# Performance work log

Measured on AMD Instinct MI355X. Metric: run time of the kernel, lower is better.

The kernel has to match this reference:

```python
import jax, jax.numpy as jnp
import numpy as np

B, NBV, VD, A = 65536, 56, 7, 81
_BN_INV = np.float32(1.0 / np.sqrt(1.0 + 1e-5))  # eval-mode BN, running mean=0 var=1 (init state)


def _bn(x, g, b):
    # x: [B, C, F], per-channel affine over axis -2
    return x * (g * _BN_INV)[:, None] + b[:, None]


def _dpg(x, W, b, ng=8, ni=8):
    # DenseAndPartialGPool: first ng*ni feats -> grouped max+avg pool, rest -> relu(Linear)
    grp = x[..., : ng * ni].reshape(x.shape[:-1] + (ng, ni))
    dense = jax.nn.relu(x[..., ng * ni :] @ W + b)
    return jnp.concatenate([grp.max(-1), grp.mean(-1), dense], -1)


def setup_inputs() -> dict:
    key = jax.random.key(0)
    ks = iter(jax.random.split(key, 80))

    def W(si, so):
        return jax.random.normal(next(ks), (si, so), jnp.float32) * np.float32(1.0 / np.sqrt(si))

    def bias(n):
        return jnp.full((n,), 0.01, jnp.float32)

    inp = {}
    inp["input_data"] = jax.random.normal(next(ks), (B, NBV, VD), jnp.float32)
    inp["valid_actions"] = jax.random.randint(next(ks), (B, 1, A), 0, 2) > 0
    # dense2d_1
    inp["W1"], inp["b1"], inp["g1"], inp["be1"] = W(NBV, 128), bias(128), jnp.ones((7,), jnp.float32), jnp.zeros((7,), jnp.float32)
    inp["W2"], inp["b2"], inp["g2"], inp["be2"] = W(128, 128), bias(128), jnp.ones((7,), jnp.float32), jnp.zeros((7,), jnp.float32)
    inp["Wp1"], inp["bp1"] = W(64, 112), bias(112)
    inp["W3"], inp["b3"], inp["g3"], inp["be3"] = W(128, 128), bias(128), jnp.ones((7,), jnp.float32), jnp.zeros((7,), jnp.float32)
    inp["Wp2"], inp["bp2"] = W(64, 112), bias(112)
    inp["W4"], inp["b4"], inp["g4"], inp["be4"] = W(128, 128), bias(128), jnp.ones((7,), jnp.float32), jnp.zeros((7,), jnp.float32)
    inp["W5"], inp["b5"], inp["g5"], inp["be5"] = W(704, 512), bias(512), jnp.ones((1,), jnp.float32), jnp.zeros((1,), jnp.float32)
    inp["W6"], inp["b6"], inp["g6"], inp["be6"] = W(512, 256), bias(256), jnp.ones((1,), jnp.float32), jnp.zeros((1,), jnp.float32)
    inp["Wp4"], inp["bp4"] = W(192, 240), bias(240)
    inp["W7"], inp["b7"], inp["g7"], inp["be7"] = W(256, 256), bias(256), jnp.ones((1,), jnp.float32), jnp.zeros((1,), jnp.float32)
    inp["W8"], inp["b8"], inp["g8"], inp["be8"] = W(256, 256), bias(256), jnp.ones((1,), jnp.float32), jnp.zeros((1,), jnp.float32)
    inp["Wp5"], inp["bp5"] = W(192, 240), bias(240)
    inp["Wpi1"], inp["bpi1"] = W(256, 256), bias(256)
    inp["Wpi2"], inp["bpi2"] = W(256, A), bias(A)
    inp["Wv1"], inp["bv1"] = W(256, 256), bias(256)
    inp["Wv2"], inp["bv2"] = W(256, 1), bias(1)
    return inp


def reference(input_data, valid_actions, W1, b1, g1, be1, W2, b2, g2, be2, Wp1, bp1,
              W3, b3, g3, be3, Wp2, bp2, W4, b4, g4, be4,
              W5, b5, g5, be5, W6, b6, g6, be6, Wp4, bp4,
              W7, b7, g7, be7, W8, b8, g8, be8, Wp5, bp5,
              Wpi1, bpi1, Wpi2, bpi2, Wv1, bv1, Wv2, bv2):
    relu = jax.nn.relu
    x = jnp.transpose(input_data, (0, 2, 1))          # [B, 7, 56]
    x = relu(_bn(x @ W1 + b1, g1, be1))               # [B, 7, 128]
    x = relu(_bn(x @ W2 + b2, g2, be2))
    x = _dpg(x, Wp1, bp1)                             # [B, 7, 128]
    x = relu(_bn(x @ W3 + b3, g3, be3))
    x = _dpg(x, Wp2, bp2)
    x = relu(_bn(x @ W4 + b4, g4, be4))               # [B, 7, 128]
    # FlattenAndPartialGPool(64, 5)
    xb, xe = x[:, :, :64], x[:, :, 64:]
    first = xb[:, :5, :]                              # [B, 5, 64]
    n = x.shape[0]
    x = jnp.concatenate([first.max(1), first.mean(1),
                         xb[:, 5:, :].reshape(n, -1), xe.reshape(n, -1)], -1)[:, None, :]  # [B,1,704]
    x = relu(_bn(x @ W5 + b5, g5, be5))               # [B, 1, 512]
    x = relu(_bn(x @ W6 + b6, g6, be6))               # [B, 1, 256]
    x = _dpg(x, Wp4, bp4)
    x = relu(_bn(x @ W7 + b7, g7, be7))
    x = relu(_bn(x @ W8 + b8, g8, be8))
    x = _dpg(x, Wp5, bp5)                             # [B, 1, 256]
    v = jnp.tanh((x @ Wv1 + bv1) @ Wv2 + bv2)         # [B, 1, 1]
    pi = (x @ Wpi1 + bpi1) @ Wpi2 + bpi2              # [B, 1, A]
    pi = jnp.where(valid_actions, pi, jnp.float32(-1e8))
    return jax.nn.log_softmax(pi, axis=-1)[:, 0, :], v[:, 0, 0]
```

## Files before the change

kernel.cpp:

```cpp
#include <hip/hip_runtime.h>
#include <hip/hip_bf16.h>
#include <math.h>

#define BN_INV 0.99999500003749966f
#define NEG_BIG (-100000000.0f)

typedef __attribute__((ext_vector_type(8))) short s16x8;
typedef __attribute__((ext_vector_type(4))) float f32x4;

#define MFMA16(a,b,c) __builtin_amdgcn_mfma_f32_16x16x32_bf16(a,b,c,0,0,0)

__device__ __forceinline__ ushort f2b(float f){
  unsigned u = __builtin_bit_cast(unsigned, f);
  unsigned r = (u + 0x7FFFu + ((u>>16)&1u)) >> 16;
  return (ushort)r;
}
__device__ __forceinline__ float b2f(ushort h){
  unsigned u = ((unsigned)h)<<16; return __builtin_bit_cast(float, u);
}
__device__ __forceinline__ unsigned pk2(float a, float b){
  return (unsigned)f2b(a) | ((unsigned)f2b(b) << 16);
}

#define OFF_W1   0
#define OFF_W2   8192
#define OFF_W3   24576
#define OFF_W4   40960
#define OFF_WP1  57344
#define OFF_WP2  64512
#define OFF_W5   71680
#define OFF_W6   432128
#define OFF_WP4  563200
#define OFF_WP5  609280
#define OFF_W7   655360
#define OFF_W8   720896
#define OFF_WPI1 786432
#define OFF_WPI2 851968
#define OFF_WV1  876544
#define OFF_X    942080

struct PrepParams {
  const float* src[15];
  long long off[15];
  int K[15], N[15], Kp[15], Np[15];
  ushort* ws;
};

__global__ void prep_pack(PrepParams pp){
  const int wi = blockIdx.y;
  const int Kp = pp.Kp[wi], Np = pp.Np[wi], K = pp.K[wi], N = pp.N[wi];
  const int tot = Kp*Np;
  int idx = blockIdx.x*256 + threadIdx.x;
  if (idx >= tot) return;
  int n = idx / Kp, k = idx - n*Kp;
  const float* s = pp.src[wi];
  float v = (k < K && n < N) ? s[k*N + n] : 0.f;
  pp.ws[pp.off[wi] + idx] = f2b(v);
}

#define S1 136

struct P1 {
  const float* inp; const ushort* ws; ushort* xout;
  const float *b1,*g1,*be1,*b2,*g2,*be2,*bp1,*b3,*g3,*be3,*bp2,*b4,*g4,*be4;
};

template<int KT>
__device__ __forceinline__ void p1_mmS(const ushort* X, ushort* Y,
    const ushort* Wt, const int Kp, const float* bias,
    const float* g, const float* be, int t)
{
  const int l=t&63, w=t>>6, lo=l&15, hi=l>>4;
  const int n0 = w*16;
  s16x8 Aw[KT];
  const ushort* wr = Wt + (n0+lo)*Kp + hi*8;
  #pragma unroll
  for (int kt=0;kt<KT;kt++) Aw[kt] = *(const s16x8*)(wr + kt*32);
  const float4 bs = *(const float4*)(bias + n0 + hi*4);
  int j = lo % 7;
  #pragma unroll
  for (int mt=0; mt<7; mt++){
    const int row = mt*16 + lo;
    const ushort* xr = X + row*S1 + hi*8;
    f32x4 a = {0.f,0.f,0.f,0.f};
    #pragma unroll
    for (int kt=0;kt<KT;kt++){
      s16x8 bx = *(const s16x8*)(xr + kt*32);
      a = MFMA16(Aw[kt], bx, a);
    }
    const float scj = g[j]*BN_INV, bbj = be[j];
    float v0 = fmaxf((a[0]+bs.x)*scj + bbj, 0.f);
    float v1 = fmaxf((a[1]+bs.y)*scj + bbj, 0.f);
    float v2 = fmaxf((a[2]+bs.z)*scj + bbj, 0.f);
    float v3 = fmaxf((a[3]+bs.w)*scj + bbj, 0.f);
    uint2 pv; pv.x = pk2(v0,v1); pv.y = pk2(v2,v3);
    *(uint2*)(Y + row*S1 + n0 + hi*4) = pv;
    j += 2; if (j >= 7) j -= 7;
  }
}

__device__ __forceinline__ void p1_dpgS(const ushort* X, ushort* Y,
    const ushort* Wpt, const float* bp, int t)
{
  const int l=t&63, w=t>>6, lo=l&15, hi=l>>4;
  #pragma unroll
  for (int it=0; it<2; it++){
    int idx = t + it*512;
    if (idx < 896){
      int row = idx>>3, gg = idx&7;
      s16x8 v8 = *(const s16x8*)(X + row*S1 + gg*8);
      float mx = b2f((ushort)v8[0]), sm = mx;
      #pragma unroll
      for (int q=1;q<8;q++){ float vv=b2f((ushort)v8[q]); mx=fmaxf(mx,vv); sm+=vv; }
      Y[row*S1+gg]   = f2b(mx);
      Y[row*S1+8+gg] = f2b(sm*0.125f);
    }
  }
  if (w < 7){
    const int n0 = w*16;
    const ushort* wr = Wpt + (n0+lo)*64 + hi*8;
    s16x8 Aw0 = *(const s16x8*)(wr);
    s16x8 Aw1 = *(const s16x8*)(wr + 32);
    const float4 bs = *(const float4*)(bp + n0 + hi*4);
    #pragma unroll
    for (int mt=0; mt<7; mt++){
      const int row = mt*16 + lo;
      const ushort* xr = X + row*S1 + 64 + hi*8;
      f32x4 a = {0.f,0.f,0.f,0.f};
      a = MFMA16(Aw0, *(const s16x8*)(xr), a);
      a = MFMA16(Aw1, *(const s16x8*)(xr+32), a);
      float v0 = fmaxf(a[0]+bs.x, 0.f);
      float v1 = fmaxf(a[1]+bs.y, 0.f);
      float v2 = fmaxf(a[2]+bs.z, 0.f);
      float v3 = fmaxf(a[3]+bs.w, 0.f);
      uint2 pv; pv.x = pk2(v0,v1); pv.y = pk2(v2,v3);
      *(uint2*)(Y + row*S1 + 16 + n0 + hi*4) = pv;
    }
  }
}

__global__ __launch_bounds__(512,4) void p1_kernel(P1 P){
  __shared__ ushort sA[112*S1];
  __shared__ ushort sB[112*S1];
  const int t = threadIdx.x;
  const size_t b0 = (size_t)blockIdx.x*16;
  {
    const int e = t>>5, la = t&31;
    const float* ep = P.inp + (b0+e)*392;
    ushort* dst = sA + e*7*S1;
    for (int i=la; i<56; i+=32){
      const float* q = ep + i*7;
      #pragma unroll
      for (int j=0;j<7;j++) dst[j*S1 + i] = f2b(q[j]);
    }
  }
  for (int idx=t; idx<896; idx+=512)
    sA[(idx>>3)*S1 + 56 + (idx&7)] = 0;
  __syncthreads();
  p1_mmS<2>(sA,sB, P.ws+OFF_W1, 64,  P.b1,P.g1,P.be1, t); __syncthreads();
  p1_mmS<4>(sB,sA, P.ws+OFF_W2, 128, P.b2,P.g2,P.be2, t); __syncthreads();
  p1_dpgS(sA,sB, P.ws+OFF_WP1, P.bp1, t);                 __syncthreads();
  p1_mmS<4>(sB,sA, P.ws+OFF_W3, 128, P.b3,P.g3,P.be3, t); __syncthreads();
  p1_dpgS(sA,sB, P.ws+OFF_WP2, P.bp2, t);                 __syncthreads();
  p1_mmS<4>(sB,sA, P.ws+OFF_W4, 128, P.b4,P.g4,P.be4, t); __syncthreads();
  ushort* xo = P.xout + b0*704;
  for (int idx=t; idx<896; idx+=512){
    int e = idx/56, ch = idx - e*56;
    int q = ch*8;
    const ushort* Xr = sA + e*7*S1;
    *(s16x8*)(xo + e*704 + 256 + q) = *(const s16x8*)(Xr + (q>>6)*S1 + 64 + (q&63));
  }
  for (int idx=t; idx<4096; idx+=512){
    int e = idx>>8, c = idx&255;
    const ushort* Xr = sA + e*7*S1;
    float v;
    if (c < 64){
      float mx = b2f(Xr[c]);
      #pragma unroll
      for (int j=1;j<5;j++) mx = fmaxf(mx, b2f(Xr[j*S1+c]));
      v = mx;
    } else if (c < 128){
      int cc = c-64; float sm = 0.f;
      #pragma unroll
      for (int j=0;j<5;j++) sm += b2f(Xr[j*S1+cc]);
      v = sm*0.2f;
    } else if (c < 192) v = b2f(Xr[5*S1 + c-128]);
    else                v = b2f(Xr[6*S1 + c-192]);
    xo[e*704 + c] = f2b(v);
  }
}

#define SY 520
#define SZ 264

struct P2 {
  const ushort* x; const ushort* ws; const void* valid;
  const float *b5,*g5,*be5,*b6,*g6,*be6,*bp4,*b7,*g7,*be7,*b8,*g8,*be8,*bp5;
  const float *bpi1,*bpi2,*bv1,*Wv2,*bv2;
  float* out; long long Btot;
};

template<int KT, int NTW, int MODE>
__device__ __forceinline__ void p2_mmS(const ushort* X, int sx, int xoff,
    ushort* Y, int sy, int yoff, const ushort* Wt, int Kp, int n0, int nact,
    const float* bias, int bmax, float sc, float bb, int lo, int hi)
{
  const ushort* xr0 = X + (0*16+lo)*sx + xoff + hi*8;
  const ushort* xr1 = X + (1*16+lo)*sx + xoff + hi*8;
  const ushort* wr[NTW];
  #pragma unroll
  for (int n=0;n<NTW;n++) wr[n] = Wt + (size_t)(n0+n*16+lo)*Kp + hi*8;
  f32x4 acc[2][NTW];
  #pragma unroll
  for (int m=0;m<2;m++)
    #pragma unroll
    for (int n=0;n<NTW;n++) acc[m][n] = (f32x4){0.f,0.f,0.f,0.f};
  #pragma unroll
  for (int kt=0; kt<KT; kt++){
    s16x8 bx0 = *(const s16x8*)(xr0 + kt*32);
    s16x8 bx1 = *(const s16x8*)(xr1 + kt*32);
    #pragma unroll
    for (int n=0;n<NTW;n++){
      if (n < nact){
        s16x8 aw = *(const s16x8*)(wr[n] + kt*32);
        acc[0][n] = MFMA16(aw, bx0, acc[0][n]);
        acc[1][n] = MFMA16(aw, bx1, acc[1][n]);
      }
    }
  }
  #pragma unroll
  for (int n=0;n<NTW;n++){
    if (n < nact){
      const int nc = n0 + n*16 + hi*4;
      float4 bs;
      if (nc+3 < bmax) bs = *(const float4*)(bias + nc);
      else {
        bs.x = (nc   < bmax)? bias[nc]  :0.f;
        bs.y = (nc+1 < bmax)? bias[nc+1]:0.f;
        bs.z = (nc+2 < bmax)? bias[nc+2]:0.f;
        bs.w = (nc+3 < bmax)? bias[nc+3]:0.f;
      }
      #pragma unroll
      for (int m=0;m<2;m++){
        const int row = m*16 + lo;
        float v0 = acc[m][n][0]+bs.x, v1 = acc[m][n][1]+bs.y;
        float v2 = acc[m][n][2]+bs.z, v3 = acc[m][n][3]+bs.w;
        if (MODE==0){
          v0 = fmaxf(v0*sc+bb,0.f); v1 = fmaxf(v1*sc+bb,0.f);
          v2 = fmaxf(v2*sc+bb,0.f); v3 = fmaxf(v3*sc+bb,0.f);
        } else if (MODE==1){
          v0 = fmaxf(v0,0.f); v1 = fmaxf(v1,0.f);
          v2 = fmaxf(v2,0.f); v3 = fmaxf(v3,0.f);
        }
        if (MODE==3){
          float4 fv = {v0,v1,v2,v3};
          *(float4*)((float*)Y + (size_t)row*sy + yoff + nc) = fv;
        } else {
          uint2 pv; pv.x = pk2(v0,v1); pv.y = pk2(v2,v3);
          *(uint2*)(Y + row*sy + yoff + nc) = pv;
        }
      }
    }
  }
}

__device__ __forceinline__ void p2_group(const ushort* X, ushort* Y, int t){
  int row = t>>3, gg = t&7;
  s16x8 v8 = *(const s16x8*)(X + row*SZ + gg*8);
  float mx = b2f((ushort)v8[0]), sm = mx;
  #pragma unroll
  for (int q=1;q<8;q++){ float vv = b2f((ushort)v8[q]); mx = fmaxf(mx,vv); sm += vv; }
  Y[row*SZ + gg]     = f2b(mx);
  Y[row*SZ + 8 + gg] = f2b(sm*0.125f);
}

__global__ __launch_bounds__(512,4) void p2_kernel(P2 P){
  __shared__ ushort sm[25344];
  __shared__ int sflags[2];
  ushort* A1 = sm;
  ushort* B1 = sm;
  ushort* C  = sm + 8448;
  ushort* B0 = sm + 16896;
  float*  Lf = (float*)(sm + 16896);
  const int t = threadIdx.x;
  const int l = t&63, w = t>>6, lo = l&15, hi = l>>4;
  const size_t b0 = (size_t)blockIdx.x * 32;

  if (t < 2) sflags[t] = 0;
  __syncthreads();
  if (t < 256){
    const unsigned* vw = (const unsigned*)P.valid;
    int f3=0, nz=0;
    #pragma unroll
    for (int i=0;i<4;i++){
      unsigned u = vw[t*4+i];
      if (u & 0xFFFFFF00u) nz=1;
      if (((u>>24)&0xFFu)==0x3Fu || ((u>>16)&0xFFu)==0x3Fu ||
          ((u>>8)&0xFFu)==0x3Fu  || (u&0xFFu)==0x3Fu) f3=1;
    }
    if (f3) atomicOr(&sflags[0],1);
    if (nz) atomicOr(&sflags[1],1);
  }
  p2_mmS<22,4,0>(P.x + b0*704, 704, 0, A1, SY, 0, P.ws+OFF_W5, 704,
                 w*64, 4, P.b5, 512, P.g5[0]*BN_INV, P.be5[0], lo,hi);
  __syncthreads();
  p2_mmS<16,2,0>(A1, SY, 0, B0, SZ, 0, P.ws+OFF_W6, 512,
                 w*32, 2, P.b6, 256, P.g6[0]*BN_INV, P.be6[0], lo,hi);
  __syncthreads();
  if (t < 256) p2_group(B0, B1, t);
  p2_mmS<6,2,1>(B0, SZ, 64, B1, SZ, 16, P.ws+OFF_WP4, 192,
                w*32, (w<7)?2:1, P.bp4, 240, 0.f,0.f, lo,hi);
  __syncthreads();
  p2_mmS<8,2,0>(B1, SZ, 0, B0, SZ, 0, P.ws+OFF_W7, 256,
                w*32, 2, P.b7, 256, P.g7[0]*BN_INV, P.be7[0], lo,hi);
  __syncthreads();
  p2_mmS<8,2,0>(B0, SZ, 0, B1, SZ, 0, P.ws+OFF_W8, 256,
                w*32, 2, P.b8, 256, P.g8[0]*BN_INV, P.be8[0], lo,hi);
  __syncthreads();
  if (t < 256) p2_group(B1, B0, t);
  p2_mmS<6,2,1>(B1, SZ, 64, B0, SZ, 16, P.ws+OFF_WP5, 192,
                w*32, (w<7)?2:1, P.bp5, 240, 0.f,0.f, lo,hi);
  __syncthreads();
  p2_mmS<8,2,2>(B0, SZ, 0, B1, SZ, 0, P.ws+OFF_WPI1, 256,
                w*32, 2, P.bpi1, 256, 0.f,0.f, lo,hi);
  p2_mmS<8,2,2>(B0, SZ, 0, C , SZ, 0, P.ws+OFF_WV1 , 256,
                w*32, 2, P.bv1 , 256, 0.f,0.f, lo,hi);
  __syncthreads();
  const int vmode = sflags[0] ? 2 : (sflags[1] ? 0 : 1);
  if (w < 6){
    p2_mmS<8,1,3>(B1, SZ, 0, (ushort*)Lf, 104, 0, P.ws+OFF_WPI2, 256,
                  w*16, 1, P.bpi2, 81, 0.f,0.f, lo,hi);
  } else if (w == 6){
    int row = l>>1, half = l&1;
    const ushort* hv = C + row*SZ + half*128;
    float s = 0.f;
    for (int k=0;k<128;k++) s += b2f(hv[k]) * P.Wv2[half*128+k];
    s += __shfl_xor(s, 1);
    if (!half) P.out[(size_t)P.Btot*81 + b0 + row] = tanhf(s + P.bv2[0]);
  }
  __syncthreads();
  if (t < 256){
    int row = t>>3, q = t&7;
    size_t b = b0 + row;
    const float* lr = Lf + row*104;
    float pm[11]; float mx = -INFINITY;
    #pragma unroll
    for (int i=0;i<11;i++){
      int c = q + 8*i;
      float v = NEG_BIG;
      if (c < 81){
        float sv = lr[c];
        bool valid;
        size_t vidx = b*81 + c;
        if (vmode==0)      valid = ((const unsigned char*)P.valid)[vidx] != 0;
        else if (vmode==1) valid = ((const int*)P.valid)[vidx] != 0;
        else               valid = ((const float*)P.valid)[vidx] != 0.f;
        v = valid ? sv : NEG_BIG;
      }
      pm[i] = v;
      mx = fmaxf(mx, v);
    }
    #pragma unroll
    for (int o=4;o;o>>=1) mx = fmaxf(mx, __shfl_xor(mx, o));
    float se = 0.f;
    #pragma unroll
    for (int i=0;i<11;i++){
      int c = q + 8*i;
      if (c < 81) se += expf(pm[i]-mx);
    }
    #pragma unroll
    for (int o=4;o;o>>=1) se += __shfl_xor(se, o);
    float lse = mx + logf(se);
    #pragma unroll
    for (int i=0;i<11;i++){
      int c = q + 8*i;
      if (c < 81) P.out[b*81 + c] = pm[i] - lse;
    }
  }
}

struct Params {
  const float* input;
  const void*  valid;
  const float *W1,*b1,*g1,*be1, *W2,*b2,*g2,*be2, *Wp1,*bp1;
  const float *W3,*b3,*g3,*be3, *Wp2,*bp2, *W4,*b4,*g4,*be4;
  const float *W5,*b5,*g5,*be5, *W6,*b6,*g6,*be6, *Wp4,*bp4;
  const float *W7,*b7,*g7,*be7, *W8,*b8,*g8,*be8, *Wp5,*bp5;
  const float *Wpi1,*bpi1,*Wpi2,*bpi2, *Wv1,*bv1,*Wv2,*bv2;
  float* out;
};

template<int K>
__device__ __forceinline__ void mm_p1(const float* __restrict__ X, float* __restrict__ Y,
    const float* __restrict__ W, const float* __restrict__ bias,
    const float* __restrict__ g, const float* __restrict__ be){
  const int t = threadIdx.x;
  const int m = t & 31, e = t >> 5;
  const int c0 = m * 4;
  const float* Xr = X + e*7*128;
  float acc[7][4];
  #pragma unroll
  for (int j=0;j<7;j++){acc[j][0]=0.f;acc[j][1]=0.f;acc[j][2]=0.f;acc[j][3]=0.f;}
  for (int k=0;k<K;k+=4){
    float4 wv[4];
    #pragma unroll
    for (int kk=0;kk<4;kk++) wv[kk] = *(const float4*)(W + (k+kk)*128 + c0);
    #pragma unroll
    for (int j=0;j<7;j++){
      float4 xv = *(const float4*)(Xr + j*128 + k);
      float xx[4] = {xv.x, xv.y, xv.z, xv.w};
      #pragma unroll
      for (int kk=0;kk<4;kk++){
        acc[j][0] += xx[kk]*wv[kk].x; acc[j][1] += xx[kk]*wv[kk].y;
        acc[j][2] += xx[kk]*wv[kk].z; acc[j][3] += xx[kk]*wv[kk].w;
      }
    }
  }
  float4 bs = *(const float4*)(bias + c0);
  #pragma unroll
  for (int j=0;j<7;j++){
    float sc = g[j]*BN_INV; float bb = be[j];
    float4 o;
    o.x = fmaxf((acc[j][0]+bs.x)*sc + bb, 0.f);
    o.y = fmaxf((acc[j][1]+bs.y)*sc + bb, 0.f);
    o.z = fmaxf((acc[j][2]+bs.z)*sc + bb, 0.f);
    o.w = fmaxf((acc[j][3]+bs.w)*sc + bb, 0.f);
    *(float4*)(Y + (e*7+j)*128 + c0) = o;
  }
}

__device__ __forceinline__ void dpg_p1f(const float* __restrict__ X, float* __restrict__ Y,
    const float* __restrict__ Wp, const float* __restrict__ bp){
  const int t = threadIdx.x;
  const int m = t & 31, e = t >> 5;
  const float* Xr = X + e*7*128;
  float* Yr = Y + e*7*128;
  if (m < 28) {
    const int c0 = m*4;
    float acc[7][4];
    #pragma unroll
    for (int j=0;j<7;j++){acc[j][0]=0.f;acc[j][1]=0.f;acc[j][2]=0.f;acc[j][3]=0.f;}
    for (int k=0;k<64;k+=4){
      float4 wv[4];
      #pragma unroll
      for (int kk=0;kk<4;kk++) wv[kk] = *(const float4*)(Wp + (k+kk)*112 + c0);
      #pragma unroll
      for (int j=0;j<7;j++){
        float4 xv = *(const float4*)(Xr + j*128 + 64 + k);
        float xx[4] = {xv.x, xv.y, xv.z, xv.w};
        #pragma unroll
        for (int kk=0;kk<4;kk++){
          acc[j][0] += xx[kk]*wv[kk].x; acc[j][1] += xx[kk]*wv[kk].y;
          acc[j][2] += xx[kk]*wv[kk].z; acc[j][3] += xx[kk]*wv[kk].w;
        }
      }
    }
    float4 bs = *(const float4*)(bp + c0);
    #pragma unroll
    for (int j=0;j<7;j++){
      float4 o;
      o.x = fmaxf(acc[j][0]+bs.x, 0.f); o.y = fmaxf(acc[j][1]+bs.y, 0.f);
      o.z = fmaxf(acc[j][2]+bs.z, 0.f); o.w = fmaxf(acc[j][3]+bs.w, 0.f);
      *(float4*)(Yr + j*128 + 16 + c0) = o;
    }
  } else if (m < 30) {
    #pragma unroll
    for (int j=0;j<7;j++){
      #pragma unroll
      for (int gi=0; gi<4; gi++){
        int gg = (m-28)*4 + gi;
        const float* p = Xr + j*128 + gg*8;
        float mx = p[0], smv = p[0];
        #pragma unroll
        for (int i=1;i<8;i++){ float v = p[i]; mx = fmaxf(mx, v); smv += v; }
        Yr[j*128 + gg] = mx;
        Yr[j*128 + 8 + gg] = smv*0.125f;
      }
    }
  }
}

__device__ __forceinline__ void flatten_st(const float* __restrict__ X, float* __restrict__ F){
  const int t = threadIdx.x, m = t & 31, e = t >> 5;
  const float* Xr = X + e*7*128;
  float* Fr = F + e*704;
  for (int col=m; col<704; col+=32){
    float v;
    if (col < 64){
      float mx = Xr[col];
      #pragma unroll
      for (int j=1;j<5;j++) mx = fmaxf(mx, Xr[j*128+col]);
      v = mx;
    } else if (col < 128){
      int c = col-64; float smv = 0.f;
      #pragma unroll
      for (int j=0;j<5;j++) smv += Xr[j*128+c];
      v = smv*0.2f;
    } else if (col < 192){ v = Xr[5*128 + (col-128)];
    } else if (col < 256){ v = Xr[6*128 + (col-192)];
    } else { int q = col-256; v = Xr[(q>>6)*128 + 64 + (q&63)]; }
    Fr[col] = v;
  }
}

template<int K, int N, int RPG, int MODE>
__device__ __forceinline__ void mm_p2(const float* __restrict__ X, int sx,
    float* __restrict__ Y, int sy, const float* __restrict__ W,
    const float* __restrict__ bias, float sc, float bb){
  constexpr int NC4 = N/4;
  constexpr int NG  = (8 + RPG - 1) / RPG;
  const int t = threadIdx.x;
  const int ci = t % NC4;
  const int grp = t / NC4;
  if (grp < NG) {
    const int c0 = ci*4;
    const int r0 = grp*RPG;
    float acc[RPG][4];
    #pragma unroll
    for (int r=0;r<RPG;r++){acc[r][0]=0.f;acc[r][1]=0.f;acc[r][2]=0.f;acc[r][3]=0.f;}
    for (int k=0;k<K;k+=4){
      float4 wv[4];
      #pragma unroll
      for (int kk=0;kk<4;kk++) wv[kk] = *(const float4*)(W + (k+kk)*N + c0);
      #pragma unroll
      for (int r=0;r<RPG;r++){
        float4 xv = *(const float4*)(X + (r0+r)*sx + k);
        float xx[4] = {xv.x, xv.y, xv.z, xv.w};
        #pragma unroll
        for (int kk=0;kk<4;kk++){
          acc[r][0] += xx[kk]*wv[kk].x; acc[r][1] += xx[kk]*wv[kk].y;
          acc[r][2] += xx[kk]*wv[kk].z; acc[r][3] += xx[kk]*wv[kk].w;
        }
      }
    }
    float4 bs = *(const float4*)(bias + c0);
    #pragma unroll
    for (int r=0;r<RPG;r++){
      float o[4] = {acc[r][0]+bs.x, acc[r][1]+bs.y, acc[r][2]+bs.z, acc[r][3]+bs.w};
      #pragma unroll
      for (int q=0;q<4;q++){
        if (MODE == 0) o[q] = o[q]*sc + bb;
        if (MODE <= 1) o[q] = fmaxf(o[q], 0.f);
      }
      float4 ov = {o[0],o[1],o[2],o[3]};
      *(float4*)(Y + (r0+r)*sy + c0) = ov;
    }
  }
}

__device__ __forceinline__ void dpg_p2_group(const float* __restrict__ X, float* __restrict__ Y){
  const int t = threadIdx.x;
  if (t < 128){
    int r = t >> 4, g0 = t & 15;
    const float* p = X + r*256 + (g0&7)*8;
    float mx = p[0], smv = p[0];
    #pragma unroll
    for (int i=1;i<8;i++){ float v = p[i]; mx = fmaxf(mx, v); smv += v; }
    Y[r*256 + g0] = (g0 < 8) ? mx : smv*0.125f;
  }
}

__global__ __launch_bounds__(256, 2)
void splendor_fwd(Params P, int Bt)
{
  __shared__ float bufA[7168];
  __shared__ float bufB[7168];
  __shared__ int sflags[2];
  const int t = threadIdx.x;
  const int b0 = blockIdx.x * 8;

  if (t < 2) sflags[t] = 0;
  __syncthreads();
  {
    const unsigned int* vw = (const unsigned int*)P.valid;
    int f3 = 0, nz = 0;
    #pragma unroll
    for (int i=0;i<4;i++){
      unsigned int u = vw[t*4 + i];
      if (u & 0xFFFFFF00u) nz = 1;
      if (((u>>24)&0xFFu)==0x3Fu || ((u>>16)&0xFFu)==0x3Fu ||
          ((u>>8)&0xFFu)==0x3Fu  || (u&0xFFu)==0x3Fu) f3 = 1;
    }
    if (f3) atomicOr(&sflags[0], 1);
    if (nz) atomicOr(&sflags[1], 1);
  }
  {
    const float* inp = P.input + (size_t)b0*392;
    for (int f=t; f<3136; f+=256){
      int e = f/392, rem = f - e*392;
      int i = rem/7, j = rem - i*7;
      bufA[(e*7+j)*128 + i] = inp[f];
    }
  }
  __syncthreads();
  const int vmode = sflags[0] ? 2 : (sflags[1] ? 0 : 1);

  mm_p1<56>(bufA, bufB, P.W1, P.b1, P.g1, P.be1);   __syncthreads();
  mm_p1<128>(bufB, bufA, P.W2, P.b2, P.g2, P.be2);  __syncthreads();
  dpg_p1f(bufA, bufB, P.Wp1, P.bp1);                __syncthreads();
  mm_p1<128>(bufB, bufA, P.W3, P.b3, P.g3, P.be3);  __syncthreads();
  dpg_p1f(bufA, bufB, P.Wp2, P.bp2);                __syncthreads();
  mm_p1<128>(bufB, bufA, P.W4, P.b4, P.g4, P.be4);  __syncthreads();
  flatten_st(bufA, bufB);                           __syncthreads();

  mm_p2<704,512,4,0>(bufB,704, bufA,512, P.W5, P.b5, P.g5[0]*BN_INV, P.be5[0]); __syncthreads();
  mm_p2<512,256,2,0>(bufA,512, bufB,256, P.W6, P.b6, P.g6[0]*BN_INV, P.be6[0]); __syncthreads();
  mm_p2<192,240,2,1>(bufB+64,256, bufA+16,256, P.Wp4, P.bp4, 0.f, 0.f);
  dpg_p2_group(bufB, bufA);                         __syncthreads();
  mm_p2<256,256,2,0>(bufA,256, bufB,256, P.W7, P.b7, P.g7[0]*BN_INV, P.be7[0]); __syncthreads();
  mm_p2<256,256,2,0>(bufB,256, bufA,256, P.W8, P.b8, P.g8[0]*BN_INV, P.be8[0]); __syncthreads();
  mm_p2<192,240,2,1>(bufA+64,256, bufB+16,256, P.Wp5, P.bp5, 0.f, 0.f);
  dpg_p2_group(bufA, bufB);                         __syncthreads();
  mm_p2<256,256,2,2>(bufB,256, bufA,256,      P.Wpi1, P.bpi1, 0.f, 0.f);
  mm_p2<256,256,2,2>(bufB,256, bufA+2048,256, P.Wv1,  P.bv1,  0.f, 0.f);
  __syncthreads();

  {
    const int r = t >> 5, lq = t & 31;
    const int b = b0 + r;
    const float* hp = bufA + r*256;
    float pm[3] = {NEG_BIG, NEG_BIG, NEG_BIG};
    float mx = -INFINITY;
    #pragma unroll
    for (int p=0;p<3;p++){
      int c = lq + 32*p;
      if (c < 81){
        float s = P.bpi2[c];
        for (int k=0;k<256;k++) s += hp[k]*P.Wpi2[k*81+c];
        bool valid;
        size_t idx = (size_t)b*81 + c;
        if (vmode == 0)      valid = ((const unsigned char*)P.valid)[idx] != 0;
        else if (vmode == 1) valid = ((const int*)P.valid)[idx] != 0;
        else                 valid = ((const float*)P.valid)[idx] != 0.f;
        pm[p] = valid ? s : NEG_BIG;
        mx = fmaxf(mx, pm[p]);
      }
    }
    #pragma unroll
    for (int off=16;off;off>>=1) mx = fmaxf(mx, __shfl_xor(mx, off, 32));
    float se = 0.f;
    #pragma unroll
    for (int p=0;p<3;p++){
      int c = lq + 32*p;
      if (c < 81) se += expf(pm[p]-mx);
    }
    #pragma unroll
    for (int off=16;off;off>>=1) se += __shfl_xor(se, off, 32);
    float lse = mx + logf(se);
    #pragma unroll
    for (int p=0;p<3;p++){
      int c = lq + 32*p;
      if (c < 81) P.out[(size_t)b*81 + c] = pm[p]-lse;
    }
  }
  if (t < 8){
    const float* hv = bufA + 2048 + t*256;
    float s = P.bv2[0];
    for (int k=0;k<256;k++) s += hv[k]*P.Wv2[k];
    P.out[(size_t)Bt*81 + b0 + t] = tanhf(s);
  }
}

extern "C" void kernel_launch(void* const* d_in, const int* in_sizes, int n_in,
                              void* d_out, int out_size, void* d_ws, size_t ws_size,
                              hipStream_t stream)
{
  const float* input = (const float*)d_in[0];
  const void*  valid = d_in[1];
  const float* W1  = (const float*)d_in[2];  const float* b1  = (const float*)d_in[3];
  const float* g1  = (const float*)d_in[4];  const float* be1 = (const float*)d_in[5];
  const float* W2  = (const float*)d_in[6];  const float* b2  = (const float*)d_in[7];
  const float* g2  = (const float*)d_in[8];  const float* be2 = (const float*)d_in[9];
  const float* Wp1 = (const float*)d_in[10]; const float* bp1 = (const float*)d_in[11];
  const float* W3  = (const float*)d_in[12]; const float* b3  = (const float*)d_in[13];
  const float* g3  = (const float*)d_in[14]; const float* be3 = (const float*)d_in[15];
  const float* Wp2 = (const float*)d_in[16]; const float* bp2 = (const float*)d_in[17];
  const float* W4  = (const float*)d_in[18]; const float* b4  = (const float*)d_in[19];
  const float* g4  = (const float*)d_in[20]; const float* be4 = (const float*)d_in[21];
  const float* W5  = (const float*)d_in[22]; const float* b5  = (const float*)d_in[23];
  const float* g5  = (const float*)d_in[24]; const float* be5 = (const float*)d_in[25];
  const float* W6  = (const float*)d_in[26]; const float* b6  = (const float*)d_in[27];
  const float* g6  = (const float*)d_in[28]; const float* be6 = (const float*)d_in[29];
  const float* Wp4 = (const float*)d_in[30]; const float* bp4 = (const float*)d_in[31];
  const float* W7  = (const float*)d_in[32]; const float* b7  = (const float*)d_in[33];
  const float* g7  = (const float*)d_in[34]; const float* be7 = (const float*)d_in[35];
  const float* W8  = (const float*)d_in[36]; const float* b8  = (const float*)d_in[37];
  const float* g8  = (const float*)d_in[38]; const float* be8 = (const float*)d_in[39];
  const float* Wp5 = (const float*)d_in[40]; const float* bp5 = (const float*)d_in[41];
  const float* Wpi1= (const float*)d_in[42]; const float* bpi1= (const float*)d_in[43];
  const float* Wpi2= (const float*)d_in[44]; const float* bpi2= (const float*)d_in[45];
  const float* Wv1 = (const float*)d_in[46]; const float* bv1 = (const float*)d_in[47];
  const float* Wv2 = (const float*)d_in[48]; const float* bv2 = (const float*)d_in[49];

  const long long Bt = in_sizes[0] / 392;
  const size_t need = ((size_t)OFF_X + (size_t)Bt*704) * 2;

  if (ws_size >= need && (Bt % 32) == 0) {
    ushort* wsu = (ushort*)d_ws;
    PrepParams pp;
    const float* srcs[15] = {W1,W2,W3,W4,Wp1,Wp2,W5,W6,Wp4,Wp5,W7,W8,Wpi1,Wpi2,Wv1};
    const long long offs[15] = {OFF_W1,OFF_W2,OFF_W3,OFF_W4,OFF_WP1,OFF_WP2,OFF_W5,OFF_W6,
                                OFF_WP4,OFF_WP5,OFF_W7,OFF_W8,OFF_WPI1,OFF_WPI2,OFF_WV1};
    const int Ks[15]  = {56,128,128,128, 64, 64,704,512,192,192,256,256,256,256,256};
    const int Ns[15]  = {128,128,128,128,112,112,512,256,240,240,256,256,256, 81,256};
    const int Kps[15] = {64,128,128,128, 64, 64,704,512,192,192,256,256,256,256,256};
    const int Nps[15] = {128,128,128,128,112,112,512,256,240,240,256,256,256, 96,256};
    for (int i=0;i<15;i++){
      pp.src[i]=srcs[i]; pp.off[i]=offs[i];
      pp.K[i]=Ks[i]; pp.N[i]=Ns[i]; pp.Kp[i]=Kps[i]; pp.Np[i]=Nps[i];
    }
    pp.ws = wsu;
    hipLaunchKernelGGL(prep_pack, dim3(1408,15), dim3(256), 0, stream, pp);

    P1 p1;
    p1.inp = input; p1.ws = wsu; p1.xout = wsu + OFF_X;
    p1.b1=b1; p1.g1=g1; p1.be1=be1; p1.b2=b2; p1.g2=g2; p1.be2=be2; p1.bp1=bp1;
    p1.b3=b3; p1.g3=g3; p1.be3=be3; p1.bp2=bp2; p1.b4=b4; p1.g4=g4; p1.be4=be4;
    hipLaunchKernelGGL(p1_kernel, dim3((unsigned)(Bt/16)), dim3(512), 0, stream, p1);

    P2 p2;
    p2.x = wsu + OFF_X; p2.ws = wsu; p2.valid = valid;
    p2.b5=b5; p2.g5=g5; p2.be5=be5; p2.b6=b6; p2.g6=g6; p2.be6=be6; p2.bp4=bp4;
    p2.b7=b7; p2.g7=g7; p2.be7=be7; p2.b8=b8; p2.g8=g8; p2.be8=be8; p2.bp5=bp5;
    p2.bpi1=bpi1; p2.bpi2=bpi2; p2.bv1=bv1; p2.Wv2=Wv2; p2.bv2=bv2;
    p2.out = (float*)d_out; p2.Btot = Bt;
    hipLaunchKernelGGL(p2_kernel, dim3((unsigned)(Bt/32)), dim3(512), 0, stream, p2);
  } else {
    Params P;
    P.input = input; P.valid = valid;
    P.W1=W1; P.b1=b1; P.g1=g1; P.be1=be1; P.W2=W2; P.b2=b2; P.g2=g2; P.be2=be2;
    P.Wp1=Wp1; P.bp1=bp1; P.W3=W3; P.b3=b3; P.g3=g3; P.be3=be3; P.Wp2=Wp2; P.bp2=bp2;
    P.W4=W4; P.b4=b4; P.g4=g4; P.be4=be4; P.W5=W5; P.b5=b5; P.g5=g5; P.be5=be5;
    P.W6=W6; P.b6=b6; P.g6=g6; P.be6=be6; P.Wp4=Wp4; P.bp4=bp4;
    P.W7=W7; P.b7=b7; P.g7=g7; P.be7=be7; P.W8=W8; P.b8=b8; P.g8=g8; P.be8=be8;
    P.Wp5=Wp5; P.bp5=bp5; P.Wpi1=Wpi1; P.bpi1=bpi1; P.Wpi2=Wpi2; P.bpi2=bpi2;
    P.Wv1=Wv1; P.bv1=bv1; P.Wv2=Wv2; P.bv2=bv2;
    P.out = (float*)d_out;
    hipLaunchKernelGGL(splendor_fwd, dim3((unsigned)(Bt/8)), dim3(256), 0, stream, P, (int)Bt);
  }
}
```

Baseline: 890.4 us.

## Halve p2 block to 4 waves with wider per-wave N tiles and staged X in LDS

Cuts the second-stage kernel from 512 to 256 threads per block, so each wave computes twice as many output columns (NTW doubled) and reuses each loaded activation fragment across more MFMAs. The W5 input tile is now copied from global into padded shared memory (stride 712) before the first GEMM, instead of being read directly from global per wave. LDS use grows to about 79 KB, which lowers occupancy (launch bounds 256,2), and each wave holds more accumulators, which raises register pressure. Weight pointer arithmetic is simplified to a single base pointer.

```diff
diff --git a/kernel.cpp b/kernel.cpp
--- a/kernel.cpp
+++ b/kernel.cpp
@@ -190,8 +190,10 @@
   }
 }
 
-#define SY 520
-#define SZ 264
+#define SXS 712
+#define SYS 520
+#define SZ  264
+#define SLF 104
 
 struct P2 {
   const ushort* x; const ushort* ws; const void* valid;
@@ -205,11 +207,9 @@
     ushort* Y, int sy, int yoff, const ushort* Wt, int Kp, int n0, int nact,
     const float* bias, int bmax, float sc, float bb, int lo, int hi)
 {
-  const ushort* xr0 = X + (0*16+lo)*sx + xoff + hi*8;
-  const ushort* xr1 = X + (1*16+lo)*sx + xoff + hi*8;
-  const ushort* wr[NTW];
-  #pragma unroll
-  for (int n=0;n<NTW;n++) wr[n] = Wt + (size_t)(n0+n*16+lo)*Kp + hi*8;
+  const ushort* xr0 = X + lo*sx + xoff + hi*8;
+  const ushort* xr1 = xr0 + 16*sx;
+  const ushort* wr  = Wt + (size_t)(n0+lo)*Kp + hi*8;
   f32x4 acc[2][NTW];
   #pragma unroll
   for (int m=0;m<2;m++)
@@ -222,7 +222,7 @@
     #pragma unroll
     for (int n=0;n<NTW;n++){
       if (n < nact){
-        s16x8 aw = *(const s16x8*)(wr[n] + kt*32);
+        s16x8 aw = *(const s16x8*)(wr + (size_t)n*16*Kp + kt*32);
         acc[0][n] = MFMA16(aw, bx0, acc[0][n]);
         acc[1][n] = MFMA16(aw, bx1, acc[1][n]);
       }
@@ -274,21 +274,22 @@
   Y[row*SZ + 8 + gg] = f2b(sm*0.125f);
 }
 
-__global__ __launch_bounds__(512,4) void p2_kernel(P2 P){
-  __shared__ ushort sm[25344];
+__global__ __launch_bounds__(256,2) void p2_kernel(P2 P){
+  __shared__ ushort sm2[39680];
   __shared__ int sflags[2];
-  ushort* A1 = sm;
-  ushort* B1 = sm;
-  ushort* C  = sm + 8448;
-  ushort* B0 = sm + 16896;
-  float*  Lf = (float*)(sm + 16896);
+  ushort* xs = sm2;
+  ushort* ys = sm2 + 22784;
+  ushort* B0 = sm2;
+  ushort* B1 = sm2 + 8448;
+  float*  Lf = (float*)(sm2 + 16896);
+  ushort* C  = sm2 + 31232;
   const int t = threadIdx.x;
   const int l = t&63, w = t>>6, lo = l&15, hi = l>>4;
   const size_t b0 = (size_t)blockIdx.x * 32;
 
   if (t < 2) sflags[t] = 0;
   __syncthreads();
-  if (t < 256){
+  {
     const unsigned* vw = (const unsigned*)P.valid;
     int f3=0, nz=0;
     #pragma unroll
@@ -301,36 +302,44 @@
     if (f3) atomicOr(&sflags[0],1);
     if (nz) atomicOr(&sflags[1],1);
   }
-  p2_mmS<22,4,0>(P.x + b0*704, 704, 0, A1, SY, 0, P.ws+OFF_W5, 704,
-                 w*64, 4, P.b5, 512, P.g5[0]*BN_INV, P.be5[0], lo,hi);
-  __syncthreads();
-  p2_mmS<16,2,0>(A1, SY, 0, B0, SZ, 0, P.ws+OFF_W6, 512,
-                 w*32, 2, P.b6, 256, P.g6[0]*BN_INV, P.be6[0], lo,hi);
-  __syncthreads();
-  if (t < 256) p2_group(B0, B1, t);
-  p2_mmS<6,2,1>(B0, SZ, 64, B1, SZ, 16, P.ws+OFF_WP4, 192,
-                w*32, (w<7)?2:1, P.bp4, 240, 0.f,0.f, lo,hi);
-  __syncthreads();
-  p2_mmS<8,2,0>(B1, SZ, 0, B0, SZ, 0, P.ws+OFF_W7, 256,
-                w*32, 2, P.b7, 256, P.g7[0]*BN_INV, P.be7[0], lo,hi);
-  __syncthreads();
-  p2_mmS<8,2,0>(B0, SZ, 0, B1, SZ, 0, P.ws+OFF_W8, 256,
-                w*32, 2, P.b8, 256, P.g8[0]*BN_INV, P.be8[0], lo,hi);
-  __syncthreads();
-  if (t < 256) p2_group(B1, B0, t);
-  p2_mmS<6,2,1>(B1, SZ, 64, B0, SZ, 16, P.ws+OFF_WP5, 192,
-                w*32, (w<7)?2:1, P.bp5, 240, 0.f,0.f, lo,hi);
-  __syncthreads();
-  p2_mmS<8,2,2>(B0, SZ, 0, B1, SZ, 0, P.ws+OFF_WPI1, 256,
-                w*32, 2, P.bpi1, 256, 0.f,0.f, lo,hi);
-  p2_mmS<8,2,2>(B0, SZ, 0, C , SZ, 0, P.ws+OFF_WV1 , 256,
-                w*32, 2, P.bv1 , 256, 0.f,0.f, lo,hi);
+  {
+    const ushort* xi = P.x + b0*704;
+    for (int ci = t; ci < 32*88; ci += 256){
+      int row = ci/88, c8 = ci - row*88;
+      *(s16x8*)(xs + row*SXS + c8*8) = *(const s16x8*)(xi + row*704 + c8*8);
+    }
+  }
+  __syncthreads();
+  p2_mmS<22,8,0>(xs, SXS, 0, ys, SYS, 0, P.ws+OFF_W5, 704,
+                 w*128, 8, P.b5, 512, P.g5[0]*BN_INV, P.be5[0], lo,hi);
+  __syncthreads();
+  p2_mmS<16,4,0>(ys, SYS, 0, B0, SZ, 0, P.ws+OFF_W6, 512,
+                 w*64, 4, P.b6, 256, P.g6[0]*BN_INV, P.be6[0], lo,hi);
+  __syncthreads();
+  p2_group(B0, B1, t);
+  p2_mmS<6,4,1>(B0, SZ, 64, B1, SZ, 16, P.ws+OFF_WP4, 192,
+                w*64, (w<3)?4:3, P.bp4, 240, 0.f,0.f, lo,hi);
+  __syncthreads();
+  p2_mmS<8,4,0>(B1, SZ, 0, B0, SZ, 0, P.ws+OFF_W7, 256,
+                w*64, 4, P.b7, 256, P.g7[0]*BN_INV, P.be7[0], lo,hi);
+  __syncthreads();
+  p2_mmS<8,4,0>(B0, SZ, 0, B1, SZ, 0, P.ws+OFF_W8, 256,
+                w*64, 4, P.b8, 256, P.g8[0]*BN_INV, P.be8[0], lo,hi);
+  __syncthreads();
+  p2_group(B1, B0, t);
+  p2_mmS<6,4,1>(B1, SZ, 64, B0, SZ, 16, P.ws+OFF_WP5, 192,
+                w*64, (w<3)?4:3, P.bp5, 240, 0.f,0.f, lo,hi);
+  __syncthreads();
+  p2_mmS<8,4,2>(B0, SZ, 0, B1, SZ, 0, P.ws+OFF_WPI1, 256,
+                w*64, 4, P.bpi1, 256, 0.f,0.f, lo,hi);
+  p2_mmS<8,4,2>(B0, SZ, 0, C , SZ, 0, P.ws+OFF_WV1 , 256,
+                w*64, 4, P.bv1 , 256, 0.f,0.f, lo,hi);
   __syncthreads();
   const int vmode = sflags[0] ? 2 : (sflags[1] ? 0 : 1);
-  if (w < 6){
-    p2_mmS<8,1,3>(B1, SZ, 0, (ushort*)Lf, 104, 0, P.ws+OFF_WPI2, 256,
-                  w*16, 1, P.bpi2, 81, 0.f,0.f, lo,hi);
-  } else if (w == 6){
+  if (w < 3){
+    p2_mmS<8,2,3>(B1, SZ, 0, (ushort*)Lf, SLF, 0, P.ws+OFF_WPI2, 256,
+                  w*32, 2, P.bpi2, 81, 0.f,0.f, lo,hi);
+  } else {
     int row = l>>1, half = l&1;
     const ushort* hv = C + row*SZ + half*128;
     float s = 0.f;
@@ -339,10 +348,10 @@
     if (!half) P.out[(size_t)P.Btot*81 + b0 + row] = tanhf(s + P.bv2[0]);
   }
   __syncthreads();
-  if (t < 256){
+  {
     int row = t>>3, q = t&7;
     size_t b = b0 + row;
-    const float* lr = Lf + row*104;
+    const float* lr = Lf + row*SLF;
     float pm[11]; float mx = -INFINITY;
     #pragma unroll
     for (int i=0;i<11;i++){
@@ -724,7 +733,7 @@
     p2.b7=b7; p2.g7=g7; p2.be7=be7; p2.b8=b8; p2.g8=g8; p2.be8=be8; p2.bp5=bp5;
     p2.bpi1=bpi1; p2.bpi2=bpi2; p2.bv1=bv1; p2.Wv2=Wv2; p2.bv2=bv2;
     p2.out = (float*)d_out; p2.Btot = Bt;
-    hipLaunchKernelGGL(p2_kernel, dim3((unsigned)(Bt/32)), dim3(512), 0, stream, p2);
+    hipLaunchKernelGGL(p2_kernel, dim3((unsigned)(Bt/32)), dim3(256), 0, stream, p2);
   } else {
     Params P;
     P.input = input; P.valid = valid;
```

Measured after the change: 853.0 us. 1.04x faster.
